# Kernel optimization log

Hardware: AMD Instinct MI355X
Metric: run time of the kernel (lower is better)

## Reference

```python
import jax, jax.numpy as jnp
import numpy as np

DIM = 2
NX, NY = 3, 3
N_BASIS = NX * NY          # 9
K_EMB = 32
D = N_BASIS + K_EMB        # 41
K_DET = 4
SPIN_DIM = 8
HIDDEN = 64
DS = 0.01                  # delta_scale
B, N = 65536, 6

_MATCHINGS_6 = [((0,1),(2,3),(4,5)), ((0,1),(2,4),(3,5)), ((0,1),(2,5),(3,4)),
                ((0,2),(1,3),(4,5)), ((0,2),(1,4),(3,5)), ((0,2),(1,5),(3,4)),
                ((0,3),(1,2),(4,5)), ((0,3),(1,4),(2,5)), ((0,3),(1,5),(2,4)),
                ((0,4),(1,2),(3,5)), ((0,4),(1,3),(2,5)), ((0,4),(1,5),(2,3)),
                ((0,5),(1,2),(3,4)), ((0,5),(1,3),(2,4)), ((0,5),(1,4),(2,3))]

def _matching_signs():
    signs = []
    for m in _MATCHINGS_6:
        perm = [i for pair in m for i in pair]
        inv = sum(1 for a in range(6) for b in range(a + 1, 6) if perm[a] > perm[b])
        signs.append((-1) ** inv)
    return np.array(signs, np.float32)

_M = np.array(_MATCHINGS_6, np.int32)          # (15,3,2)
_II = jnp.asarray(_M[:, :, 0])                  # (15,3)
_JJ = jnp.asarray(_M[:, :, 1])                  # (15,3)
_SG = jnp.asarray(_matching_signs())            # (15,)


def ho_basis_1d(t, n_max):
    """1D harmonic-oscillator eigenfunctions psi_0..psi_{n_max-1}. t:(...)->(...,n_max)."""
    psi0 = (jnp.pi ** -0.25) * jnp.exp(-0.5 * t * t)
    psis = [psi0]
    if n_max > 1:
        psis.append(jnp.sqrt(2.0) * t * psi0)
    for n in range(2, n_max):
        psis.append(jnp.sqrt(2.0 / n) * t * psis[-1] - jnp.sqrt((n - 1) / n) * psis[-2])
    return jnp.stack(psis, axis=-1)


def setup_inputs() -> dict:
    key = jax.random.key(0)
    ks = jax.random.split(key, 16)
    x = jax.random.normal(ks[0], (B, N, DIM), jnp.float32)
    spin = jax.random.randint(ks[1], (B, N), 0, 2)
    in_dim = DIM + SPIN_DIM
    spin_embed = 0.1 * jax.random.normal(ks[2], (2, SPIN_DIM), jnp.float32)
    W1 = jax.random.normal(ks[3], (in_dim, HIDDEN), jnp.float32) / np.sqrt(in_dim)
    b1 = 0.01 * jax.random.normal(ks[4], (HIDDEN,), jnp.float32)
    W2 = jax.random.normal(ks[5], (HIDDEN, HIDDEN), jnp.float32) / np.sqrt(HIDDEN)
    b2 = 0.01 * jax.random.normal(ks[6], (HIDDEN,), jnp.float32)
    W3 = 0.1 * jax.random.normal(ks[7], (HIDDEN, K_EMB), jnp.float32) / np.sqrt(HIDDEN)
    b3 = 0.01 * jax.random.normal(ks[8], (K_EMB,), jnp.float32)
    # HF projector buffer
    C_occ = 0.3 * jax.random.normal(ks[9], (N_BASIS, 3), jnp.float32)
    P_hf = jnp.zeros((D, D), jnp.float32).at[:N_BASIS, :N_BASIS].set(C_occ @ C_occ.T)
    dF_ud = jax.random.normal(ks[10], (K_DET, D, D), jnp.float32)
    dF_uu = jax.random.normal(ks[11], (K_DET, D, D), jnp.float32)
    dF_dd = jax.random.normal(ks[12], (K_DET, D, D), jnp.float32)
    w = jax.random.normal(ks[13], (K_DET,), jnp.float32)
    return {"x": x, "spin": spin, "spin_embed": spin_embed, "W1": W1, "b1": b1,
            "W2": W2, "b2": b2, "W3": W3, "b3": b3, "P_hf": P_hf,
            "dF_ud": dF_ud, "dF_uu": dF_uu, "dF_dd": dF_dd, "w": w}


def reference(x, spin, spin_embed, W1, b1, W2, b2, W3, b3, P_hf, dF_ud, dF_uu, dF_dd, w):
    Bc, Nc, _ = x.shape
    # 2D HO basis: product of 1D Hermite functions -> (B,N,NX*NY)
    px = ho_basis_1d(x[..., 0], NX)
    py = ho_basis_1d(x[..., 1], NY)
    Phi = (px[..., :, None] * py[..., None, :]).reshape(Bc, Nc, NX * NY)
    # learned embedding MLP (2 SiLU layers + linear head)
    inp = jnp.concatenate([x, spin_embed[spin]], axis=-1)      # (B,N,2+spin_dim)
    hdd = jax.nn.silu(inp @ W1 + b1)
    hdd = jax.nn.silu(hdd @ W2 + b2)
    h_learned = hdd @ W3 + b3
    h = jnp.concatenate([Phi, h_learned], axis=-1)             # (B,N,D)
    # spin-sector masks
    is_up = spin == 0
    is_dn = spin == 1
    f = h.dtype
    uu = (is_up[:, :, None] & is_up[:, None, :]).astype(f)
    dd = (is_dn[:, :, None] & is_dn[:, None, :]).astype(f)
    ud = (is_up[:, :, None] & is_dn[:, None, :]).astype(f)
    du = (is_dn[:, :, None] & is_up[:, None, :]).astype(f)
    # pairing matrices for all K_det channels at once
    F_uu = DS * (dF_uu - jnp.swapaxes(dF_uu, 1, 2))            # (K,D,D)
    F_dd = DS * (dF_dd - jnp.swapaxes(dF_dd, 1, 2))
    P0 = jnp.concatenate([P_hf[None], jnp.zeros((K_DET - 1, D, D), f)], axis=0)
    F_ud = P0 + DS * dF_ud
    A_uu = jnp.einsum('bnd,kde,bme->kbnm', h, F_uu, h)
    A_dd = jnp.einsum('bnd,kde,bme->kbnm', h, F_dd, h)
    A_ud = jnp.einsum('bnd,kde,bme->kbnm', h, F_ud, h)
    A = A_uu * uu + A_dd * dd + A_ud * ud - jnp.swapaxes(A_ud, -1, -2) * du  # (K,B,6,6)
    # Pfaffian via 15 perfect matchings, vectorized over K and B
    terms = A[:, :, _II, _JJ]                                   # (K,B,15,3)
    pfs = jnp.einsum('kbm,m->kb', terms.prod(axis=-1), _SG)     # (K,B)
    total = jnp.einsum('kb,k->b', pfs, w)                       # (B,)
    sign = jnp.sign(total)
    sign = jnp.where(sign == 0, jnp.ones_like(sign), sign)
    logabs = 0.5 * jnp.log(total * total + 1e-60)
    return sign, logabs
```

## Files before the change

### kernel.cpp

```cpp
#include <hip/hip_runtime.h>

#define B_TOT 65536
#define RS 44
#define KDET 4

#define OFF_W2T  0
#define OFF_W3T  4352
#define OFF_SC   6528
#define SC_STRIDE 1584
#define LDS_FLOATS (6528 + 4*1584)

#define WS_F   0

__device__ const int PN_TAB[15] = {0,0,0,0,0,1,1,1,1,2,2,2,3,3,4};
__device__ const int PM_TAB[15] = {1,2,3,4,5,2,3,4,5,3,4,5,4,5,5};
__device__ const int M1_TAB[15] = {0,0,0,1,1,1,2,2,2,3,3,3,4,4,4};
__device__ const int M2_TAB[15] = {9,10,11,6,7,8,5,7,8,5,6,8,5,6,7};
__device__ const int M3_TAB[15] = {14,13,12,14,13,12,14,11,10,13,11,9,12,10,9};

__device__ __forceinline__ float bcastf(float v, int l) {
    return __int_as_float(__builtin_amdgcn_readlane(__float_as_int(v), l));
}
#define WFENCE() asm volatile("s_waitcnt lgkmcnt(0)" ::: "memory")

__global__ void prep_F(const float* __restrict__ dFud, const float* __restrict__ dFuu,
                       const float* __restrict__ dFdd, const float* __restrict__ Phf,
                       float4* __restrict__ ws)
{
    int t = blockIdx.x * 256 + threadIdx.x;
    if (t >= 12*11*64) return;
    int d  = t & 63;
    int c  = (t >> 6) % 11;
    int sk = t / (11*64);
    int s = sk >> 2, k = sk & 3;
    const float* src = (s==0) ? dFuu : (s==1) ? dFdd : dFud;
    float v[4];
    #pragma unroll
    for (int j=0;j<4;j++){
        int e = 4*c + j;
        float r = 0.f;
        if (d < 41 && e < 41) {
            if (s < 2) r = 0.01f * (src[(k*41+d)*41+e] - src[(k*41+e)*41+d]);
            else     { r = 0.01f *  src[(k*41+d)*41+e]; if (k==0) r += Phf[d*41+e]; }
        }
        v[j] = r;
    }
    ws[WS_F + t] = make_float4(v[0],v[1],v[2],v[3]);
}

__global__ __launch_bounds__(256, 3)
void pfaff_main(const float* __restrict__ x, const int* __restrict__ spin,
                const float* __restrict__ se, const float* __restrict__ W1,
                const float* __restrict__ b1, const float* __restrict__ W2,
                const float* __restrict__ b2, const float* __restrict__ W3,
                const float* __restrict__ b3, const float* __restrict__ wdet,
                const float4* __restrict__ ws, float* __restrict__ out)
{
    __shared__ __align__(16) float lds[LDS_FLOATS];
    float* W2tl = lds + OFF_W2T;
    float* W3tl = lds + OFF_W3T;

    const int tid  = threadIdx.x;
    const int wave = tid >> 6, lane = tid & 63;

    for (int idx = tid; idx < 64*68; idx += 256) {
        int j = idx / 68, i = idx - j*68;
        W2tl[idx] = (i < 64) ? W2[i*64 + j] : 0.f;
    }
    for (int idx = tid; idx < 32*68; idx += 256) {
        int j = idx / 68, i = idx - j*68;
        W3tl[idx] = (i < 64) ? W3[i*32 + j] : 0.f;
    }
    float* sc  = lds + OFF_SC + wave*SC_STRIDE;
    float* t_s = sc;
    float* h1  = sc + 128;
    float* hA  = sc + 1056;
    for (int i = lane; i < SC_STRIDE; i += 64) sc[i] = 0.f;
    __syncthreads();

    const float4* wsF = ws + WS_F;

    const float b1r = b1[lane];
    const float b2r = b2[lane];
    const float b3r = b3[lane & 31];
    const float w1c0 = W1[lane], w1c1 = W1[64 + lane];
    float emb0 = 0.f, emb1 = 0.f;
    #pragma unroll
    for (int j=0;j<8;j++){
        float wv = W1[(2+j)*64 + lane];
        emb0 = fmaf(wv, se[j],   emb0);
        emb1 = fmaf(wv, se[8+j], emb1);
    }
    int pn=0, pm=0, m1i=0, m2i=0, m3i=0;
    const int p = lane & 31, g = lane >> 5;
    if (p < 15) { pn=PN_TAB[p]; pm=PM_TAB[p];
                  m1i=M1_TAB[p]; m2i=M2_TAB[p]; m3i=M3_TAB[p]; }
    float wreg[4];
    #pragma unroll
    for (int k=0;k<4;k++) wreg[k] = wdet[k];

    const int ebase = ((int)blockIdx.x * 4 + wave) * 8;
    #pragma unroll 1
    for (int pi = 0; pi < 4; ++pi) {
        const int e0 = ebase + pi*2;

        int s_n = 0; float xx = 0.f, xy = 0.f;
        if (lane < 12) {
            int gg = lane >= 6;
            int eg = e0 + gg;
            int n  = lane - gg*6;
            float2 xv = *(const float2*)(x + (size_t)(eg*6 + n)*2);
            xx = xv.x; xy = xv.y;
            s_n = spin[eg*6 + n];
        }
        unsigned long long bal = __ballot(lane < 12 && s_n == 1);
        const unsigned dn0 = (unsigned)__builtin_amdgcn_readfirstlane((int)((unsigned)bal & 63u));
        const unsigned dn1 = (unsigned)__builtin_amdgcn_readfirstlane((int)((unsigned)(bal >> 6) & 63u));

        if (lane < 12) {
            float ex = __expf(-0.5f*(xx*xx));
            float px0 = 0.7511255444649425f * ex;
            float px1 = 1.4142135623730951f * xx * px0;
            float px2 = fmaf(xx, px1, -0.7071067811865476f * px0);
            float ey = __expf(-0.5f*(xy*xy));
            float py0 = 0.7511255444649425f * ey;
            float py1 = 1.4142135623730951f * xy * py0;
            float py2 = fmaf(xy, py1, -0.7071067811865476f * py0);
            float* hr = hA + lane*RS;
            hr[0]=px0*py0; hr[1]=px0*py1; hr[2]=px0*py2;
            hr[3]=px1*py0; hr[4]=px1*py1; hr[5]=px1*py2;
            hr[6]=px2*py0; hr[7]=px2*py1; hr[8]=px2*py2;
            hr[41]=0.f; hr[42]=0.f; hr[43]=0.f;
        }

        #pragma unroll
        for (int r=0;r<12;r++){
            float xr = bcastf(xx, r);
            float yr = bcastf(xy, r);
            int   sr = __builtin_amdgcn_readlane(s_n, r);
            float a  = fmaf(xr, w1c0, b1r);
            a = fmaf(yr, w1c1, a);
            a += sr ? emb1 : emb0;
            h1[r*64 + lane] = __fdividef(a, 1.f + __expf(-a));
        }
        WFENCE();

        float acc[12];
        #pragma unroll
        for (int r=0;r<12;r++) acc[r] = b2r;
        #pragma unroll
        for (int i4=0;i4<16;i4++){
            float4 w4 = *(const float4*)(W2tl + lane*68 + i4*4);
            #pragma unroll
            for (int r=0;r<12;r++){
                float4 h4 = *(const float4*)(h1 + r*64 + i4*4);
                acc[r]=fmaf(w4.x,h4.x,acc[r]); acc[r]=fmaf(w4.y,h4.y,acc[r]);
                acc[r]=fmaf(w4.z,h4.z,acc[r]); acc[r]=fmaf(w4.w,h4.w,acc[r]);
            }
        }
        WFENCE();
        #pragma unroll
        for (int r=0;r<12;r++){
            float v = acc[r];
            h1[r*64 + lane] = __fdividef(v, 1.f + __expf(-v));
        }
        WFENCE();

        {
            int j2 = lane & 31, hf = lane >> 5;
            float a3[6];
            #pragma unroll
            for (int rr=0;rr<6;rr++) a3[rr] = b3r;
            #pragma unroll
            for (int i4=0;i4<16;i4++){
                float4 w4 = *(const float4*)(W3tl + j2*68 + i4*4);
                #pragma unroll
                for (int rr=0;rr<6;rr++){
                    float4 h4 = *(const float4*)(h1 + (hf*6+rr)*64 + i4*4);
                    a3[rr]=fmaf(w4.x,h4.x,a3[rr]); a3[rr]=fmaf(w4.y,h4.y,a3[rr]);
                    a3[rr]=fmaf(w4.z,h4.z,a3[rr]); a3[rr]=fmaf(w4.w,h4.w,a3[rr]);
                }
            }
            #pragma unroll
            for (int rr=0;rr<6;rr++) hA[(hf*6+rr)*RS + 9 + j2] = a3[rr];
        }
        WFENCE();

        float total = 0.f;
        #pragma unroll 1
        for (int k = 0; k < KDET; ++k) {
            #pragma unroll 1
            for (int pass=0; pass<3; ++pass) {
                const float4* Fp = wsF + (size_t)(pass*4 + k)*(11*64) + lane;
                float4 fA=Fp[0],    fB=Fp[64],   fC=Fp[2*64], fD=Fp[3*64];
                float4 fE=Fp[4*64], fF=Fp[5*64], fG=Fp[6*64], fH=Fp[7*64];
                float4 fI=Fp[8*64], fJ=Fp[9*64], fK=Fp[10*64];
                const int dstb = (pass==2) ? 6 : 0;
                #pragma unroll
                for (int gg=0; gg<2; ++gg){
                    const unsigned dng = gg ? dn1 : dn0;
                    const unsigned mk  = pass ? dng : ((~dng) & 63u);
                    #pragma unroll
                    for (int m=0;m<6;m++){
                        if ((mk>>m)&1) {
                            const float* hm = hA + (gg*6+m)*RS;
                            float4 q;
                            float a0, a1, a2, a3v;
                            q = *(const float4*)(hm);
                            a0  = fA.x*q.x; a1 = fA.y*q.y;
                            a2  = fA.z*q.z; a3v= fA.w*q.w;
                            q = *(const float4*)(hm+4);
                            a0=fmaf(fB.x,q.x,a0); a1=fmaf(fB.y,q.y,a1);
                            a2=fmaf(fB.z,q.z,a2); a3v=fmaf(fB.w,q.w,a3v);
                            q = *(const float4*)(hm+8);
                            a0=fmaf(fC.x,q.x,a0); a1=fmaf(fC.y,q.y,a1);
                            a2=fmaf(fC.z,q.z,a2); a3v=fmaf(fC.w,q.w,a3v);
                            q = *(const float4*)(hm+12);
                            a0=fmaf(fD.x,q.x,a0); a1=fmaf(fD.y,q.y,a1);
                            a2=fmaf(fD.z,q.z,a2); a3v=fmaf(fD.w,q.w,a3v);
                            q = *(const float4*)(hm+16);
                            a0=fmaf(fE.x,q.x,a0); a1=fmaf(fE.y,q.y,a1);
                            a2=fmaf(fE.z,q.z,a2); a3v=fmaf(fE.w,q.w,a3v);
                            q = *(const float4*)(hm+20);
                            a0=fmaf(fF.x,q.x,a0); a1=fmaf(fF.y,q.y,a1);
                            a2=fmaf(fF.z,q.z,a2); a3v=fmaf(fF.w,q.w,a3v);
                            q = *(const float4*)(hm+24);
                            a0=fmaf(fG.x,q.x,a0); a1=fmaf(fG.y,q.y,a1);
                            a2=fmaf(fG.z,q.z,a2); a3v=fmaf(fG.w,q.w,a3v);
                            q = *(const float4*)(hm+28);
                            a0=fmaf(fH.x,q.x,a0); a1=fmaf(fH.y,q.y,a1);
                            a2=fmaf(fH.z,q.z,a2); a3v=fmaf(fH.w,q.w,a3v);
                            q = *(const float4*)(hm+32);
                            a0=fmaf(fI.x,q.x,a0); a1=fmaf(fI.y,q.y,a1);
                            a2=fmaf(fI.z,q.z,a2); a3v=fmaf(fI.w,q.w,a3v);
                            q = *(const float4*)(hm+36);
                            a0=fmaf(fJ.x,q.x,a0); a1=fmaf(fJ.y,q.y,a1);
                            a2=fmaf(fJ.z,q.z,a2); a3v=fmaf(fJ.w,q.w,a3v);
                            q = *(const float4*)(hm+40);
                            a0=fmaf(fK.x,q.x,a0); a1=fmaf(fK.y,q.y,a1);
                            a2=fmaf(fK.z,q.z,a2); a3v=fmaf(fK.w,q.w,a3v);
                            float t = (a0+a1)+(a2+a3v);
                            if (lane < RS)
                                t_s[(gg*12 + dstb + m)*RS + lane] = (lane < 41) ? t : 0.f;
                        }
                    }
                }
            }
            WFENCE();

            float av = 0.f;
            if (p < 15) {
                unsigned dng = g ? dn1 : dn0;
                int sn = (int)((dng>>pn)&1), sm = (int)((dng>>pm)&1);
                int hrow, trow; float sg;
                if (sn == sm)      { hrow = pn; trow = pm;     sg =  1.f; }
                else if (sn == 0)  { hrow = pn; trow = 6 + pm; sg =  1.f; }
                else               { hrow = pm; trow = 6 + pn; sg = -1.f; }
                const float4* hp = (const float4*)(hA  + (g*6  + hrow)*RS);
                const float4* tp = (const float4*)(t_s + (g*12 + trow)*RS);
                float a0=0.f,a1=0.f,a2=0.f,a3v=0.f;
                #pragma unroll
                for (int q=0;q<11;q++){
                    float4 hv = hp[q]; float4 tv = tp[q];
                    a0=fmaf(hv.x,tv.x,a0); a1=fmaf(hv.y,tv.y,a1);
                    a2=fmaf(hv.z,tv.z,a2); a3v=fmaf(hv.w,tv.w,a3v);
                }
                av = sg * ((a0+a1)+(a2+a3v));
            }
            int g32 = lane & 32;
            float q1 = __shfl(av, g32 + m1i);
            float q2 = __shfl(av, g32 + m2i);
            float q3 = __shfl(av, g32 + m3i);
            float term = 0.f;
            if (p < 15) { float pr = q1*q2*q3; term = (p & 1) ? -pr : pr; }
            term += __shfl_xor(term, 1);
            term += __shfl_xor(term, 2);
            term += __shfl_xor(term, 4);
            term += __shfl_xor(term, 8);
            total = fmaf(wreg[k], term, total);
            WFENCE();
        }

        if (p == 0) {
            int e = e0 + g;
            float sgn = (total > 0.f) ? 1.f : ((total < 0.f) ? -1.f : 1.f);
            out[e]         = sgn;
            out[B_TOT + e] = 0.5f * logf(fmaf(total, total, 1e-60f));
        }
        WFENCE();
    }
}

extern "C" void kernel_launch(void* const* d_in, const int* in_sizes, int n_in,
                              void* d_out, int out_size, void* d_ws, size_t ws_size,
                              hipStream_t stream)
{
    const float* x    = (const float*)d_in[0];
    const int*   spin = (const int*)  d_in[1];
    const float* se   = (const float*)d_in[2];
    const float* W1   = (const float*)d_in[3];
    const float* b1   = (const float*)d_in[4];
    const float* W2   = (const float*)d_in[5];
    const float* b2   = (const float*)d_in[6];
    const float* W3   = (const float*)d_in[7];
    const float* b3   = (const float*)d_in[8];
    const float* Phf  = (const float*)d_in[9];
    const float* dFud = (const float*)d_in[10];
    const float* dFuu = (const float*)d_in[11];
    const float* dFdd = (const float*)d_in[12];
    const float* w    = (const float*)d_in[13];
    float* out = (float*)d_out;
    float4* ws = (float4*)d_ws;

    hipLaunchKernelGGL(prep_F, dim3(33), dim3(256), 0, stream,
                       dFud, dFuu, dFdd, Phf, ws);
    hipLaunchKernelGGL(pfaff_main, dim3(2048), dim3(256), 0, stream,
                       x, spin, se, W1, b1, W2, b2, W3, b3, w, ws, out);
}
```

Measured before the change: 397.0 us.

## Stream W2/W3 from prepacked global buffers instead of LDS, shrink per-block work

The prep kernel now also repacks W2 and W3 into float4-interleaved global workspace layouts. The main kernel reads those weights straight from global or cache instead of staging transposed copies in LDS. This removes the per-block weight transpose and the __syncthreads, and cuts LDS use so more blocks fit per CU (launch bounds raised to 4). Each block now handles half as many samples over twice as many blocks, and the zero-padded last F column chunk is trimmed to a scalar FMA. In exchange, the MLP inner loops take global-memory latency per float4 and lose full unrolling.

Result: slower. 495.1 us (+24.7%).

```diff
diff --git a/kernel.cpp b/kernel.cpp
--- a/kernel.cpp
+++ b/kernel.cpp
@@ -4,13 +4,13 @@
 #define RS 44
 #define KDET 4
 
-#define OFF_W2T  0
-#define OFF_W3T  4352
-#define OFF_SC   6528
 #define SC_STRIDE 1584
-#define LDS_FLOATS (6528 + 4*1584)
+#define LDS_FLOATS (4*SC_STRIDE)
 
 #define WS_F   0
+#define WS_W2  8448
+#define WS_W3  9472
+#define WS_TOT 9984
 
 __device__ const int PN_TAB[15] = {0,0,0,0,0,1,1,1,1,2,2,2,3,3,4};
 __device__ const int PM_TAB[15] = {1,2,3,4,5,2,3,4,5,3,4,5,4,5,5};
@@ -23,85 +23,85 @@
 }
 #define WFENCE() asm volatile("s_waitcnt lgkmcnt(0)" ::: "memory")
 
-__global__ void prep_F(const float* __restrict__ dFud, const float* __restrict__ dFuu,
-                       const float* __restrict__ dFdd, const float* __restrict__ Phf,
-                       float4* __restrict__ ws)
+__global__ void prep_all(const float* __restrict__ dFud, const float* __restrict__ dFuu,
+                         const float* __restrict__ dFdd, const float* __restrict__ Phf,
+                         const float* __restrict__ W2, const float* __restrict__ W3,
+                         float4* __restrict__ ws)
 {
     int t = blockIdx.x * 256 + threadIdx.x;
-    if (t >= 12*11*64) return;
-    int d  = t & 63;
-    int c  = (t >> 6) % 11;
-    int sk = t / (11*64);
-    int s = sk >> 2, k = sk & 3;
-    const float* src = (s==0) ? dFuu : (s==1) ? dFdd : dFud;
-    float v[4];
-    #pragma unroll
-    for (int j=0;j<4;j++){
-        int e = 4*c + j;
-        float r = 0.f;
-        if (d < 41 && e < 41) {
-            if (s < 2) r = 0.01f * (src[(k*41+d)*41+e] - src[(k*41+e)*41+d]);
-            else     { r = 0.01f *  src[(k*41+d)*41+e]; if (k==0) r += Phf[d*41+e]; }
-        }
-        v[j] = r;
+    if (t < 12*11*64) {
+        int d  = t & 63;
+        int c  = (t >> 6) % 11;
+        int sk = t / (11*64);
+        int s = sk >> 2, k = sk & 3;
+        const float* src = (s==0) ? dFuu : (s==1) ? dFdd : dFud;
+        float v[4];
+        #pragma unroll
+        for (int j=0;j<4;j++){
+            int e = 4*c + j;
+            float r = 0.f;
+            if (d < 41 && e < 41) {
+                if (s < 2) r = 0.01f * (src[(k*41+d)*41+e] - src[(k*41+e)*41+d]);
+                else     { r = 0.01f *  src[(k*41+d)*41+e]; if (k==0) r += Phf[d*41+e]; }
+            }
+            v[j] = r;
+        }
+        ws[WS_F + t] = make_float4(v[0],v[1],v[2],v[3]);
+    } else if (t < 12*11*64 + 1024) {
+        int u = t - 12*11*64;
+        int i4 = u >> 6, j = u & 63;
+        ws[WS_W2 + u] = make_float4(W2[(4*i4+0)*64 + j], W2[(4*i4+1)*64 + j],
+                                    W2[(4*i4+2)*64 + j], W2[(4*i4+3)*64 + j]);
+    } else if (t < WS_TOT) {
+        int u = t - (12*11*64 + 1024);
+        int i4 = u >> 5, j2 = u & 31;
+        ws[WS_W3 + u] = make_float4(W3[(4*i4+0)*32 + j2], W3[(4*i4+1)*32 + j2],
+                                    W3[(4*i4+2)*32 + j2], W3[(4*i4+3)*32 + j2]);
     }
-    ws[WS_F + t] = make_float4(v[0],v[1],v[2],v[3]);
 }
 
-__global__ __launch_bounds__(256, 3)
+__global__ __launch_bounds__(256, 4)
 void pfaff_main(const float* __restrict__ x, const int* __restrict__ spin,
                 const float* __restrict__ se, const float* __restrict__ W1,
-                const float* __restrict__ b1, const float* __restrict__ W2,
-                const float* __restrict__ b2, const float* __restrict__ W3,
+                const float* __restrict__ b1, const float* __restrict__ b2,
                 const float* __restrict__ b3, const float* __restrict__ wdet,
                 const float4* __restrict__ ws, float* __restrict__ out)
 {
     __shared__ __align__(16) float lds[LDS_FLOATS];
-    float* W2tl = lds + OFF_W2T;
-    float* W3tl = lds + OFF_W3T;
-
     const int tid  = threadIdx.x;
     const int wave = tid >> 6, lane = tid & 63;
-
-    for (int idx = tid; idx < 64*68; idx += 256) {
-        int j = idx / 68, i = idx - j*68;
-        W2tl[idx] = (i < 64) ? W2[i*64 + j] : 0.f;
-    }
-    for (int idx = tid; idx < 32*68; idx += 256) {
-        int j = idx / 68, i = idx - j*68;
-        W3tl[idx] = (i < 64) ? W3[i*32 + j] : 0.f;
-    }
-    float* sc  = lds + OFF_SC + wave*SC_STRIDE;
+    float* sc  = lds + wave*SC_STRIDE;
     float* t_s = sc;
     float* h1  = sc + 128;
     float* hA  = sc + 1056;
+
     for (int i = lane; i < SC_STRIDE; i += 64) sc[i] = 0.f;
-    __syncthreads();
-
-    const float4* wsF = ws + WS_F;
-
-    const float b1r = b1[lane];
-    const float b2r = b2[lane];
-    const float b3r = b3[lane & 31];
+    WFENCE();
+
+    const float4* wsF  = ws + WS_F;
+    const float4* wsW2 = ws + WS_W2;
+    const float4* wsW3 = ws + WS_W3;
+
     const float w1c0 = W1[lane], w1c1 = W1[64 + lane];
-    float emb0 = 0.f, emb1 = 0.f;
+    float emb0 = b1[lane], emb1 = emb0;
     #pragma unroll
     for (int j=0;j<8;j++){
         float wv = W1[(2+j)*64 + lane];
         emb0 = fmaf(wv, se[j],   emb0);
         emb1 = fmaf(wv, se[8+j], emb1);
     }
-    int pn=0, pm=0, m1i=0, m2i=0, m3i=0;
-    const int p = lane & 31, g = lane >> 5;
-    if (p < 15) { pn=PN_TAB[p]; pm=PM_TAB[p];
-                  m1i=M1_TAB[p]; m2i=M2_TAB[p]; m3i=M3_TAB[p]; }
-    float wreg[4];
-    #pragma unroll
-    for (int k=0;k<4;k++) wreg[k] = wdet[k];
-
-    const int ebase = ((int)blockIdx.x * 4 + wave) * 8;
+    const float b2r = b2[lane];
+    const float b3r = b3[lane & 31];
+    int pk = 0;
+    {
+        const int p_ = lane & 31;
+        if (p_ < 15) pk = PN_TAB[p_] | (PM_TAB[p_]<<5) | (M1_TAB[p_]<<10)
+                        | (M2_TAB[p_]<<15) | (M3_TAB[p_]<<20);
+    }
+
+    const int ebase = ((int)blockIdx.x * 4 + wave) * 4;
     #pragma unroll 1
-    for (int pi = 0; pi < 4; ++pi) {
+    for (int pi = 0; pi < 2; ++pi) {
         const int e0 = ebase + pi*2;
 
         int s_n = 0; float xx = 0.f, xy = 0.f;
@@ -138,9 +138,8 @@
             float xr = bcastf(xx, r);
             float yr = bcastf(xy, r);
             int   sr = __builtin_amdgcn_readlane(s_n, r);
-            float a  = fmaf(xr, w1c0, b1r);
+            float a  = fmaf(xr, w1c0, (sr ? emb1 : emb0));
             a = fmaf(yr, w1c1, a);
-            a += sr ? emb1 : emb0;
             h1[r*64 + lane] = __fdividef(a, 1.f + __expf(-a));
         }
         WFENCE();
@@ -148,9 +147,9 @@
         float acc[12];
         #pragma unroll
         for (int r=0;r<12;r++) acc[r] = b2r;
-        #pragma unroll
+        #pragma unroll 1
         for (int i4=0;i4<16;i4++){
-            float4 w4 = *(const float4*)(W2tl + lane*68 + i4*4);
+            float4 w4 = wsW2[i4*64 + lane];
             #pragma unroll
             for (int r=0;r<12;r++){
                 float4 h4 = *(const float4*)(h1 + r*64 + i4*4);
@@ -171,9 +170,9 @@
             float a3[6];
             #pragma unroll
             for (int rr=0;rr<6;rr++) a3[rr] = b3r;
-            #pragma unroll
+            #pragma unroll 1
             for (int i4=0;i4<16;i4++){
-                float4 w4 = *(const float4*)(W3tl + j2*68 + i4*4);
+                float4 w4 = wsW3[i4*32 + j2];
                 #pragma unroll
                 for (int rr=0;rr<6;rr++){
                     float4 h4 = *(const float4*)(h1 + (hf*6+rr)*64 + i4*4);
@@ -194,7 +193,8 @@
                 const float4* Fp = wsF + (size_t)(pass*4 + k)*(11*64) + lane;
                 float4 fA=Fp[0],    fB=Fp[64],   fC=Fp[2*64], fD=Fp[3*64];
                 float4 fE=Fp[4*64], fF=Fp[5*64], fG=Fp[6*64], fH=Fp[7*64];
-                float4 fI=Fp[8*64], fJ=Fp[9*64], fK=Fp[10*64];
+                float4 fI=Fp[8*64], fJ=Fp[9*64];
+                const float fK0 = *((const float*)(Fp + 10*64));
                 const int dstb = (pass==2) ? 6 : 0;
                 #pragma unroll
                 for (int gg=0; gg<2; ++gg){
@@ -236,9 +236,7 @@
                             q = *(const float4*)(hm+36);
                             a0=fmaf(fJ.x,q.x,a0); a1=fmaf(fJ.y,q.y,a1);
                             a2=fmaf(fJ.z,q.z,a2); a3v=fmaf(fJ.w,q.w,a3v);
-                            q = *(const float4*)(hm+40);
-                            a0=fmaf(fK.x,q.x,a0); a1=fmaf(fK.y,q.y,a1);
-                            a2=fmaf(fK.z,q.z,a2); a3v=fmaf(fK.w,q.w,a3v);
+                            a0 = fmaf(fK0, hm[40], a0);
                             float t = (a0+a1)+(a2+a3v);
                             if (lane < RS)
                                 t_s[(gg*12 + dstb + m)*RS + lane] = (lane < 41) ? t : 0.f;
@@ -248,6 +246,9 @@
             }
             WFENCE();
 
+            const int p = lane & 31, g = lane >> 5;
+            const int pn  =  pk        & 31;
+            const int pm  = (pk >> 5)  & 31;
             float av = 0.f;
             if (p < 15) {
                 unsigned dng = g ? dn1 : dn0;
@@ -268,21 +269,21 @@
                 av = sg * ((a0+a1)+(a2+a3v));
             }
             int g32 = lane & 32;
-            float q1 = __shfl(av, g32 + m1i);
-            float q2 = __shfl(av, g32 + m2i);
-            float q3 = __shfl(av, g32 + m3i);
+            float q1 = __shfl(av, g32 + ((pk >> 10) & 31));
+            float q2 = __shfl(av, g32 + ((pk >> 15) & 31));
+            float q3 = __shfl(av, g32 + ((pk >> 20) & 31));
             float term = 0.f;
             if (p < 15) { float pr = q1*q2*q3; term = (p & 1) ? -pr : pr; }
             term += __shfl_xor(term, 1);
             term += __shfl_xor(term, 2);
             term += __shfl_xor(term, 4);
             term += __shfl_xor(term, 8);
-            total = fmaf(wreg[k], term, total);
+            total = fmaf(wdet[k], term, total);
             WFENCE();
         }
 
-        if (p == 0) {
-            int e = e0 + g;
+        if ((lane & 31) == 0) {
+            int e = e0 + (lane >> 5);
             float sgn = (total > 0.f) ? 1.f : ((total < 0.f) ? -1.f : 1.f);
             out[e]         = sgn;
             out[B_TOT + e] = 0.5f * logf(fmaf(total, total, 1e-60f));
@@ -312,8 +313,8 @@
     float* out = (float*)d_out;
     float4* ws = (float4*)d_ws;
 
-    hipLaunchKernelGGL(prep_F, dim3(33), dim3(256), 0, stream,
-                       dFud, dFuu, dFdd, Phf, ws);
-    hipLaunchKernelGGL(pfaff_main, dim3(2048), dim3(256), 0, stream,
-                       x, spin, se, W1, b1, W2, b2, W3, b3, w, ws, out);
+    hipLaunchKernelGGL(prep_all, dim3(39), dim3(256), 0, stream,
+                       dFud, dFuu, dFdd, Phf, W2, W3, ws);
+    hipLaunchKernelGGL(pfaff_main, dim3(4096), dim3(256), 0, stream,
+                       x, spin, se, W1, b1, b2, b3, w, ws, out);
 }
```
